# Kernel optimization log

Hardware: AMD Instinct MI355X
Metric: run time of the kernel (lower is better)

## Reference

```python
import jax, jax.numpy as jnp
import numpy as np
import math

B, S, H, DK, NB = 2, 128, 4, 128, 4
D = H * DK  # 512


def setup_inputs() -> dict:
    key = jax.random.key(0)
    ks = jax.random.split(key, 24)
    g = lambda i, sh, std=1.0: jax.random.normal(ks[i], sh, jnp.float32) * std
    u = lambda i, sh: jax.random.uniform(ks[i], sh, jnp.float32)
    return {
        "x_m": g(0, (B, S, D)), "x_c": g(1, (B, S, D)),
        "b_m": g(2, (B, S, D)), "b_c": g(3, (B, S, D)),
        "bb_m": g(4, (B, NB, NB, D)), "bb_c": u(5, (B, NB, NB, D)),
        "p_m": g(6, (B, S, D)), "p_c": u(7, (B, S, D)),
        "W_xm": g(8, (3, D, H, DK), 0.02), "W_xc": g(9, (3, D, H, DK), 0.02),
        "W_bm": g(10, (3, D, H, DK), 0.02), "W_bc": g(11, (3, D, H, DK), 0.02),
        "Wq1_w": g(12, (DK, DK), 0.05), "Wq1_b": g(13, (DK,), 0.02),
        "Wq2_w": g(14, (DK, DK), 0.05), "Wq2_b": g(15, (DK,), 0.02),
        "Wk1_w": g(16, (DK, DK), 0.05), "Wk1_b": g(17, (DK,), 0.02),
        "Wk2_w": g(18, (DK, DK), 0.05), "Wk2_b": g(19, (DK,), 0.02),
        "mean_w": g(20, (D, D), 0.02), "mean_b": jnp.zeros((D,), jnp.float32),
        "cov_w": g(21, (D, D), 0.02), "cov_b": jnp.zeros((D,), jnp.float32),
        "ln_w": jnp.ones((D,), jnp.float32), "ln_b": jnp.zeros((D,), jnp.float32),
        "b_seq": jax.random.randint(ks[22], (B, S), 0, NB),
    }


def _elu1(x):
    return jax.nn.elu(x) + 1.0


def _tri_sagp(m1, m2, m3, c1, c2, c3):
    # fuse three diagonal Gaussians by product-of-Gaussians (precision-weighted)
    eps = 1e-24
    p1 = 1.0 / jnp.clip(c1, eps)
    p2 = 1.0 / jnp.clip(c2, eps)
    p3 = 1.0 / jnp.clip(c3, eps)
    c = 1.0 / (p1 + p2 + p3)
    return c * (m1 * p1 + m2 * p2 + m3 * p3), c


def _ln(x, w, b):
    m = jnp.mean(x, -1, keepdims=True)
    v = jnp.mean((x - m) ** 2, -1, keepdims=True)
    return (x - m) / jnp.sqrt(v + 1e-12) * w + b


def _forward(x_m, x_c, b_m, b_c, bb_m, bb_c, p_m, p_c,
             W_xm, W_xc, W_bm, W_bc,
             Wq1_w, Wq1_b, Wq2_w, Wq2_b, Wk1_w, Wk1_b, Wk2_w, Wk2_b,
             mean_w, mean_b, cov_w, cov_b, ln_w, ln_b, b_seq):
    Bb, Ss, Dd = x_m.shape
    Hh, Dk = W_xm.shape[2], W_xm.shape[3]
    proj = lambda x, w: jnp.einsum('bnd,dhk->bhnk', x, w)
    q1 = proj(x_m, W_xm[0]) + proj(b_m, W_bm[0])
    k1 = proj(x_m, W_xm[1]) + proj(b_m, W_bm[1])
    v1 = proj(x_m, W_xm[2]) + proj(b_m, W_bm[2])
    q2 = _elu1(proj(x_c, W_xc[0]) + proj(b_c, W_bc[0]))
    k2 = _elu1(proj(x_c, W_xc[1]) + proj(b_c, W_bc[1]))
    v2 = _elu1(proj(x_c, W_xc[2]) + proj(b_c, W_bc[2]))
    nb = bb_m.shape[1]
    # [B,NB,NB,D] -> [B,H,NB,NB,DK]
    bbm = bb_m.reshape(Bb, nb, nb, Hh, Dk).transpose(0, 3, 1, 2, 4)
    bbc = bb_c.reshape(Bb, nb, nb, Hh, Dk).transpose(0, 3, 1, 2, 4)
    # out[b,h,i,j,:] = bbm[b,h,b_seq[b,j],b_seq[b,i],:]  (matches torch advanced indexing + permute)
    gather = jax.vmap(lambda bb, seq: bb[:, seq[None, :], seq[:, None], :])
    bbm_b = gather(bbm, b_seq)  # [B,H,S,S,DK]
    bbc_b = gather(bbc, b_seq)
    pm = p_m.reshape(Bb, Ss, Hh, Dk).transpose(0, 2, 1, 3)  # [B,H,S,DK]
    pc = p_c.reshape(Bb, Ss, Hh, Dk).transpose(0, 2, 1, 3)
    lin = lambda x, w, b: x @ w.T + b
    fQm, fQc = _tri_sagp(q1[:, :, :, None, :], lin(bbm_b, Wq1_w, Wq1_b),
                         lin(pm, Wq2_w, Wq2_b)[:, :, :, None, :],
                         q2[:, :, :, None, :], bbc_b, pc[:, :, :, None, :])
    fKm, fKc = _tri_sagp(k1[:, :, None, :, :], lin(bbm_b, Wk1_w, Wk1_b),
                         lin(pm, Wk2_w, Wk2_b)[:, :, None, :, :],
                         k2[:, :, None, :, :], bbc_b, pc[:, :, None, :, :])
    eps = 1e-24
    # 2-Wasserstein^2 between diagonal Gaussians (the 1x1 matmul form reduces to this)
    w2 = jnp.sum((fQm - fKm) ** 2, -1) + jnp.sum(
        (jnp.sqrt(jnp.clip(fQc, eps)) - jnp.sqrt(jnp.clip(fKc, eps))) ** 2, -1)
    scores = -w2 / math.sqrt(Dk)  # [B,H,S,S]
    probs = jax.nn.softmax(scores, axis=-1)
    mean_ctx = jnp.einsum('bhij,bhjk->bhik', probs, v1)
    cov_ctx = jnp.einsum('bhij,bhjk->bhik', probs ** 2, v2)
    mean_ctx = mean_ctx.transpose(0, 2, 1, 3).reshape(Bb, Ss, Dd)
    cov_ctx = cov_ctx.transpose(0, 2, 1, 3).reshape(Bb, Ss, Dd)
    mean_h = _ln(mean_ctx @ mean_w.T + mean_b + x_m, ln_w, ln_b)
    cov_h = _ln(cov_ctx @ cov_w.T + cov_b + x_c, ln_w, ln_b)
    return mean_h, cov_h, probs


def reference(x_m, x_c, b_m, b_c, bb_m, bb_c, p_m, p_c,
              W_xm, W_xc, W_bm, W_bc,
              Wq1_w, Wq1_b, Wq2_w, Wq2_b, Wk1_w, Wk1_b, Wk2_w, Wk2_b,
              mean_w, mean_b, cov_w, cov_b, ln_w, ln_b, b_seq):
    return _forward(x_m, x_c, b_m, b_c, bb_m, bb_c, p_m, p_c,
                    W_xm, W_xc, W_bm, W_bc,
                    Wq1_w, Wq1_b, Wq2_w, Wq2_b, Wk1_w, Wk1_b, Wk2_w, Wk2_b,
                    mean_w, mean_b, cov_w, cov_b, ln_w, ln_b, b_seq)
```

## Files before the change

### kernel.cpp

```cpp
#include <hip/hip_runtime.h>
#include <math.h>

#define B_ 2
#define S_ 128
#define H_ 4
#define DK_ 128
#define NB_ 4
#define D_ 512
#define M_ 256

typedef __attribute__((ext_vector_type(8))) short short8;
typedef __attribute__((ext_vector_type(4))) float float4v;
typedef __attribute__((ext_vector_type(4))) unsigned short ushort4v;

__device__ __forceinline__ float elu1(float x) {
    return (x > 0.f) ? (x + 1.f) : __expf(x);
}

__device__ __forceinline__ unsigned short f2bf(float f) {
    unsigned u = __float_as_uint(f);
    unsigned r = (u + 0x7FFFu + ((u >> 16) & 1u)) >> 16;
    return (unsigned short)r;
}


union __attribute__((aligned(16))) PrepSMem {
    unsigned short tile[32][33];
    struct { float ps[2][8][128]; float wsh[2][128][33]; } c;
};

__global__ __launch_bounds__(256) void k_prep(
    const float* __restrict__ x_m, const float* __restrict__ b_m,
    const float* __restrict__ x_c, const float* __restrict__ b_c,
    const float* __restrict__ mean_w, const float* __restrict__ cov_w,
    const float* __restrict__ W_xm, const float* __restrict__ W_xc,
    const float* __restrict__ W_bm, const float* __restrict__ W_bc,
    const float* __restrict__ p_m, const float* __restrict__ bb_m,
    const float* __restrict__ Wq2, const float* __restrict__ bq2,
    const float* __restrict__ Wk2, const float* __restrict__ bk2,
    const float* __restrict__ Wq1, const float* __restrict__ bq1,
    const float* __restrict__ Wk1, const float* __restrict__ bk1,
    unsigned short* __restrict__ A_m, unsigned short* __restrict__ A_c,
    unsigned short* __restrict__ wm_bf, unsigned short* __restrict__ wc_bf,
    unsigned short* __restrict__ Wt,
    float* __restrict__ pq, float* __restrict__ pk,
    float* __restrict__ bbq, float* __restrict__ bbk)
{
    __shared__ PrepSMem sm;
    const int t = threadIdx.x;
    const int blk = blockIdx.x;
    const int u2 = t >> 7, tl = t & 127;

    {
#pragma unroll
        for (int u = 0; u < 4; ++u) {
            int cid = u * 65536 + blk * 256 + t;
            int job = cid >> 16;
            int off = (cid & 65535) * 4;
            const float* srcp;
            unsigned short* dst;
            if (job <= 1) {
                int m = off >> 10, k = off & 1023;
                if (job == 0) { srcp = (k < 512) ? (x_m + m * 512 + k) : (b_m + m * 512 + k - 512); dst = A_m; }
                else          { srcp = (k < 512) ? (x_c + m * 512 + k) : (b_c + m * 512 + k - 512); dst = A_c; }
            } else if (job == 2) { srcp = mean_w + off; dst = wm_bf; }
            else                 { srcp = cov_w + off;  dst = wc_bf; }
            float4 v = *(const float4*)srcp;
            ushort4v o;
            o.x = f2bf(v.x); o.y = f2bf(v.y); o.z = f2bf(v.z); o.w = f2bf(v.w);
            *(ushort4v*)(dst + off) = o;
        }
    }
    {
        const int tx = t & 31, ty = t >> 5;
        for (int it = 0; it < 12; ++it) {
            int tid = blk * 12 + it;
            int nt = tid & 15, kt = (tid >> 4) & 15, z = tid >> 8;
            int o = z >> 1, part = z & 1;
            const float* src;
            if (part == 0) src = (o < 3) ? (W_xm + o * 262144) : (W_xc + (o - 3) * 262144);
            else           src = (o < 3) ? (W_bm + o * 262144) : (W_bc + (o - 3) * 262144);
            __syncthreads();
#pragma unroll
            for (int u = 0; u < 4; ++u)
                sm.tile[ty + u * 8][tx] = f2bf(src[(kt * 32 + ty + u * 8) * 512 + nt * 32 + tx]);
            __syncthreads();
            unsigned short* dst = Wt + o * 524288 + part * 512;
#pragma unroll
            for (int u = 0; u < 4; ++u)
                dst[(nt * 32 + ty + u * 8) * 1024 + kt * 32 + tx] = sm.tile[tx][ty + u * 8];
        }
    }
    __syncthreads();
    if (blk < 144) {
        const int cunit = blk * 2 + u2;
        const float *src, *Wm, *bias; float* dst; int row0;
        if (cunit < 128)      { src = p_m;  Wm = Wq2; bias = bq2; dst = pq;  row0 = cunit * 8; }
        else if (cunit < 256) { src = p_m;  Wm = Wk2; bias = bk2; dst = pk;  row0 = (cunit - 128) * 8; }
        else if (cunit < 272) { src = bb_m; Wm = Wq1; bias = bq1; dst = bbq; row0 = (cunit - 256) * 8; }
        else                  { src = bb_m; Wm = Wk1; bias = bk1; dst = bbk; row0 = (cunit - 272) * 8; }

        float (*ps)[128] = sm.c.ps[u2];
        float (*wsh)[33] = sm.c.wsh[u2];
#pragma unroll
        for (int r = 0; r < 8; ++r) ps[r][tl] = src[(row0 + r) * 128 + tl];

        float acc[8];
#pragma unroll
        for (int r = 0; r < 8; ++r) acc[r] = 0.f;

        const int kc = tl & 31, kr0 = tl >> 5;
        for (int c0 = 0; c0 < 128; c0 += 32) {
            __syncthreads();
#pragma unroll 8
            for (int u = 0; u < 32; ++u)
                wsh[kr0 + u * 4][kc] = Wm[(kr0 + u * 4) * 128 + c0 + kc];
            __syncthreads();
#pragma unroll 8
            for (int k2 = 0; k2 < 32; ++k2) {
                float wvv = wsh[tl][k2];
#pragma unroll
                for (int r = 0; r < 8; ++r)
                    acc[r] = fmaf(ps[r][c0 + k2], wvv, acc[r]);
            }
        }
        float bv = bias[tl];
#pragma unroll
        for (int r = 0; r < 8; ++r) dst[(row0 + r) * 128 + tl] = acc[r] + bv;
    }
}

__global__ __launch_bounds__(256) void k_mm(
    const unsigned short* __restrict__ A_m, const unsigned short* __restrict__ A_c,
    const unsigned short* __restrict__ Wt, float* __restrict__ qkv)
{
    const int t = threadIdx.x;
    const int wid = blockIdx.x * 4 + (t >> 6);
    const int lane = t & 63;
    const int o = wid >> 9;
    const int rem = wid & 511;
    const int nt = rem & 31, mt = rem >> 5;
    const int m0 = mt * 16, n0 = nt * 16;
    const int l15 = lane & 15, quad = lane >> 4;

    const unsigned short* A = (o < 3) ? A_m : A_c;
    const unsigned short* ap = A + (m0 + l15) * 1024 + quad * 8;
    const unsigned short* bp = Wt + o * 524288 + (n0 + l15) * 1024 + quad * 8;

    float4v acc0 = {0.f, 0.f, 0.f, 0.f};
    float4v acc1 = {0.f, 0.f, 0.f, 0.f};
#pragma unroll
    for (int k0 = 0; k0 < 1024; k0 += 64) {
        short8 a0 = *(const short8*)(ap + k0);
        short8 b0 = *(const short8*)(bp + k0);
        short8 a1 = *(const short8*)(ap + k0 + 32);
        short8 b1 = *(const short8*)(bp + k0 + 32);
        acc0 = __builtin_amdgcn_mfma_f32_16x16x32_bf16(a0, b0, acc0, 0, 0, 0);
        acc1 = __builtin_amdgcn_mfma_f32_16x16x32_bf16(a1, b1, acc1, 0, 0, 0);
    }

    float* dst = qkv + o * 131072;
#pragma unroll
    for (int r = 0; r < 4; ++r) {
        float v = acc0[r] + acc1[r];
        if (o >= 3) v = elu1(v);
        dst[(m0 + quad * 4 + r) * 512 + n0 + l15] = v;
    }
}

__global__ __launch_bounds__(128) void k_fuseK(
    const float* __restrict__ qkv, const float* __restrict__ pk,
    const float* __restrict__ bbk, const float* __restrict__ bb_c,
    const float* __restrict__ p_c, const int* __restrict__ b_seq,
    float* __restrict__ fKm, float* __restrict__ fKs)
{
    const int t = threadIdx.x;
    const int j = blockIdx.x, h = blockIdx.y, b = blockIdx.z;
    const int d = h * 128 + t;
    const float eps = 1e-24f;
    const int base = (b * S_ + j) * D_ + d;
    const int sj = b_seq[b * S_ + j];

    float m1 = qkv[M_ * D_ + base];
    float c1 = qkv[4 * M_ * D_ + base];
    float m3 = pk[base];
    float c3 = p_c[base];

    float p1 = 1.f / fmaxf(c1, eps);
    float p3 = 1.f / fmaxf(c3, eps);
    float mp13 = m1 * p1 + m3 * p3;

#pragma unroll
    for (int sv = 0; sv < 4; ++sv) {
        int idx = (b * 16 + sj * 4 + sv) * 512 + d;
        float m2 = bbk[idx];
        float c2 = bb_c[idx];
        float p2 = 1.f / fmaxf(c2, eps);
        float cc = 1.f / (p1 + p2 + p3);
        int o = (((b * H_ + h) * 4 + sv) * S_ + j) * 128 + t;
        fKm[o] = cc * (mp13 + m2 * p2);
        fKs[o] = sqrtf(fmaxf(cc, eps));
    }
}

__global__ __launch_bounds__(128) void k_attn3(
    const float* __restrict__ qkv, const float* __restrict__ pq,
    const float* __restrict__ bbq, const float* __restrict__ bb_c,
    const float* __restrict__ p_c, const int* __restrict__ b_seq,
    const float* __restrict__ fKm, const float* __restrict__ fKs,
    float* __restrict__ probs_out, unsigned short* __restrict__ mctxb,
    unsigned short* __restrict__ cctxb)
{
    const int t = threadIdx.x;
    const int i = blockIdx.x, h = blockIdx.y, b = blockIdx.z;
    const float eps = 1e-24f;

    __shared__ __attribute__((aligned(16))) float qm[4 * 132];
    __shared__ __attribute__((aligned(16))) float qs[4 * 132];
    __shared__ float red[4];
    __shared__ float pr[128], pr2[128];

    const int si = b_seq[b * S_ + i];
    const int sj = b_seq[b * S_ + t];

    {
        const int d = h * 128 + t;
        const int base = (b * S_ + i) * D_ + d;
        float m1 = qkv[base];
        float c1 = qkv[3 * M_ * D_ + base];
        float m3 = pq[base];
        float c3 = p_c[base];
        float p1 = 1.f / fmaxf(c1, eps);
        float p3 = 1.f / fmaxf(c3, eps);
        float mp13 = m1 * p1 + m3 * p3;
#pragma unroll
        for (int sv = 0; sv < 4; ++sv) {
            int idx = (b * 16 + sv * 4 + si) * 512 + d;
            float m2 = bbq[idx];
            float c2 = bb_c[idx];
            float p2 = 1.f / fmaxf(c2, eps);
            float cc = 1.f / (p1 + p2 + p3);
            qm[sv * 132 + t] = cc * (mp13 + m2 * p2);
            qs[sv * 132 + t] = sqrtf(fmaxf(cc, eps));
        }
    }
    __syncthreads();

    const int krow = (((b * H_ + h) * 4 + si) * S_ + t) * 128;
    const float4* kmp = (const float4*)(fKm + krow);
    const float4* ksp = (const float4*)(fKs + krow);

    float w2 = 0.f;
#pragma unroll 4
    for (int k4 = 0; k4 < 32; ++k4) {
        float4 km = kmp[k4];
        float4 ks = ksp[k4];
        float4 m = *(const float4*)&qm[sj * 132 + k4 * 4];
        float4 s = *(const float4*)&qs[sj * 132 + k4 * 4];
        float d0 = m.x - km.x, d1 = m.y - km.y, d2 = m.z - km.z, d3 = m.w - km.w;
        float e0 = s.x - ks.x, e1 = s.y - ks.y, e2 = s.z - ks.z, e3 = s.w - ks.w;
        w2 += d0 * d0 + d1 * d1 + d2 * d2 + d3 * d3
            + e0 * e0 + e1 * e1 + e2 * e2 + e3 * e3;
    }
    float score = -w2 * 0.08838834764831845f;

    float mx = score;
#pragma unroll
    for (int off = 32; off >= 1; off >>= 1) mx = fmaxf(mx, __shfl_xor(mx, off));
    if ((t & 63) == 0) red[t >> 6] = mx;
    __syncthreads();
    mx = fmaxf(red[0], red[1]);
    float e = __expf(score - mx);
    float sm = e;
#pragma unroll
    for (int off = 32; off >= 1; off >>= 1) sm += __shfl_xor(sm, off);
    if ((t & 63) == 0) red[2 + (t >> 6)] = sm;
    __syncthreads();
    float p = e / (red[2] + red[3]);

    probs_out[((b * H_ + h) * S_ + i) * S_ + t] = p;
    pr[t] = p;
    pr2[t] = p * p;
    __syncthreads();

    const float* v1 = qkv + 2 * M_ * D_ + (b * S_) * D_ + h * 128 + t;
    const float* v2 = qkv + 5 * M_ * D_ + (b * S_) * D_ + h * 128 + t;
    float am = 0.f, ac = 0.f;
#pragma unroll 8
    for (int j = 0; j < 128; ++j) {
        am = fmaf(pr[j], v1[j * D_], am);
        ac = fmaf(pr2[j], v2[j * D_], ac);
    }
    mctxb[(b * S_ + i) * D_ + h * 128 + t] = f2bf(am);
    cctxb[(b * S_ + i) * D_ + h * 128 + t] = f2bf(ac);
}

__global__ __launch_bounds__(256) void k_fin_mm(
    const unsigned short* __restrict__ mctxb, const unsigned short* __restrict__ cctxb,
    const unsigned short* __restrict__ wm_bf, const unsigned short* __restrict__ wc_bf,
    float* __restrict__ y_m, float* __restrict__ y_c)
{
    const int t = threadIdx.x;
    const int wid = blockIdx.x * 4 + (t >> 6);
    const int lane = t & 63;
    const int mat = wid >> 9;
    const int rem = wid & 511;
    const int nt = rem & 31, mt = rem >> 5;
    const int m0 = mt * 16, n0 = nt * 16;
    const int l15 = lane & 15, quad = lane >> 4;

    const unsigned short* A = mat ? cctxb : mctxb;
    const unsigned short* Bw = mat ? wc_bf : wm_bf;
    float* y = mat ? y_c : y_m;

    const unsigned short* ap = A + (m0 + l15) * 512 + quad * 8;
    const unsigned short* bp = Bw + (n0 + l15) * 512 + quad * 8;

    float4v acc0 = {0.f, 0.f, 0.f, 0.f};
    float4v acc1 = {0.f, 0.f, 0.f, 0.f};
#pragma unroll
    for (int k0 = 0; k0 < 512; k0 += 64) {
        short8 a0 = *(const short8*)(ap + k0);
        short8 b0 = *(const short8*)(bp + k0);
        short8 a1 = *(const short8*)(ap + k0 + 32);
        short8 b1 = *(const short8*)(bp + k0 + 32);
        acc0 = __builtin_amdgcn_mfma_f32_16x16x32_bf16(a0, b0, acc0, 0, 0, 0);
        acc1 = __builtin_amdgcn_mfma_f32_16x16x32_bf16(a1, b1, acc1, 0, 0, 0);
    }
#pragma unroll
    for (int r = 0; r < 4; ++r)
        y[(m0 + quad * 4 + r) * 512 + n0 + l15] = acc0[r] + acc1[r];
}

__global__ __launch_bounds__(256) void k_ln(
    const float* __restrict__ y_m, const float* __restrict__ y_c,
    const float* __restrict__ mean_b, const float* __restrict__ cov_b,
    const float* __restrict__ x_m, const float* __restrict__ x_c,
    const float* __restrict__ ln_w, const float* __restrict__ ln_b,
    float* __restrict__ out)
{
    const int t = threadIdx.x;
    const int id = blockIdx.x;
    const int mat = id >> 8, row = id & 255;
    const float* yg = mat ? y_c : y_m;
    const float* bias = mat ? cov_b : mean_b;
    const float* res = mat ? x_c : x_m;
    const int base = row * 512;

    __shared__ float red[8];

    float y0 = yg[base + t] + bias[t] + res[base + t];
    float y1 = yg[base + 256 + t] + bias[256 + t] + res[base + 256 + t];
    float s = y0 + y1, ss = y0 * y0 + y1 * y1;
#pragma unroll
    for (int off = 32; off >= 1; off >>= 1) { s += __shfl_xor(s, off); ss += __shfl_xor(ss, off); }
    if ((t & 63) == 0) { red[t >> 6] = s; red[4 + (t >> 6)] = ss; }
    __syncthreads();
    float mu = (red[0] + red[1] + red[2] + red[3]) * (1.f / 512.f);
    float var = (red[4] + red[5] + red[6] + red[7]) * (1.f / 512.f) - mu * mu;
    float rstd = 1.f / sqrtf(var + 1e-12f);
    out[mat * 131072 + base + t] = (y0 - mu) * rstd * ln_w[t] + ln_b[t];
    out[mat * 131072 + base + 256 + t] = (y1 - mu) * rstd * ln_w[256 + t] + ln_b[256 + t];
}

extern "C" void kernel_launch(void* const* d_in, const int* in_sizes, int n_in,
                              void* d_out, int out_size, void* d_ws, size_t ws_size,
                              hipStream_t stream) {
    (void)in_sizes; (void)n_in; (void)out_size; (void)ws_size;
    const float* x_m   = (const float*)d_in[0];
    const float* x_c   = (const float*)d_in[1];
    const float* b_m   = (const float*)d_in[2];
    const float* b_c   = (const float*)d_in[3];
    const float* bb_m  = (const float*)d_in[4];
    const float* bb_c  = (const float*)d_in[5];
    const float* p_m   = (const float*)d_in[6];
    const float* p_c   = (const float*)d_in[7];
    const float* W_xm  = (const float*)d_in[8];
    const float* W_xc  = (const float*)d_in[9];
    const float* W_bm  = (const float*)d_in[10];
    const float* W_bc  = (const float*)d_in[11];
    const float* Wq1_w = (const float*)d_in[12];
    const float* Wq1_b = (const float*)d_in[13];
    const float* Wq2_w = (const float*)d_in[14];
    const float* Wq2_b = (const float*)d_in[15];
    const float* Wk1_w = (const float*)d_in[16];
    const float* Wk1_b = (const float*)d_in[17];
    const float* Wk2_w = (const float*)d_in[18];
    const float* Wk2_b = (const float*)d_in[19];
    const float* mean_w = (const float*)d_in[20];
    const float* mean_b = (const float*)d_in[21];
    const float* cov_w  = (const float*)d_in[22];
    const float* cov_b  = (const float*)d_in[23];
    const float* ln_w   = (const float*)d_in[24];
    const float* ln_b   = (const float*)d_in[25];
    const int*   b_seq  = (const int*)d_in[26];

    float* ws = (float*)d_ws;
    float* qkv = ws;
    float* pq  = ws + 786432;
    float* pk  = ws + 917504;
    float* bbq = ws + 1048576;
    float* bbk = ws + 1064960;
    float* fKm = ws + 1081344;
    float* fKs = ws + 1605632;
    float* y_m = ws + 2129920;
    float* y_c = ws + 2260992;
    unsigned short* A_m   = (unsigned short*)(ws + 2392064);
    unsigned short* A_c   = (unsigned short*)(ws + 2523136);
    unsigned short* Wt    = (unsigned short*)(ws + 2654208);
    unsigned short* wm_bf = (unsigned short*)(ws + 4227072);
    unsigned short* wc_bf = (unsigned short*)(ws + 4358144);
    unsigned short* mctxb = (unsigned short*)(ws + 4489216);
    unsigned short* cctxb = (unsigned short*)(ws + 4554752);
    float* out = (float*)d_out;

    k_prep<<<dim3(256), 256, 0, stream>>>(
        x_m, b_m, x_c, b_c, mean_w, cov_w, W_xm, W_xc, W_bm, W_bc,
        p_m, bb_m, Wq2_w, Wq2_b, Wk2_w, Wk2_b, Wq1_w, Wq1_b, Wk1_w, Wk1_b,
        A_m, A_c, wm_bf, wc_bf, Wt, pq, pk, bbq, bbk);
    k_mm<<<dim3(768), 256, 0, stream>>>(A_m, A_c, Wt, qkv);
    k_fuseK<<<dim3(128, 4, 2), 128, 0, stream>>>(
        qkv, pk, bbk, bb_c, p_c, b_seq, fKm, fKs);
    k_attn3<<<dim3(128, 4, 2), 128, 0, stream>>>(
        qkv, pq, bbq, bb_c, p_c, b_seq, fKm, fKs, out + 262144, mctxb, cctxb);
    k_fin_mm<<<dim3(256), 256, 0, stream>>>(
        mctxb, cctxb, wm_bf, wc_bf, y_m, y_c);
    k_ln<<<dim3(512), 256, 0, stream>>>(
        y_m, y_c, mean_b, cov_b, x_m, x_c, ln_w, ln_b, out);
}
```

Baseline: 191.1 us.

## Merge six kernels into one cooperative persistent kernel with grid syncs

Replaces the six separate kernel launches with a single cooperative kernel that runs each stage in grid-stride loops and separates stages with grid.sync(). The goal is to remove per-launch overhead and inter-kernel gaps, which matter for a pipeline of many small stages. In exchange, grid-wide barriers add cost. The grid is sized to fit at most two resident blocks per CU, and the attention stage now packs two 128-thread units into each 256-thread block. Both of these can change per-stage parallelism and occupancy.

```diff
diff --git a/kernel.cpp b/kernel.cpp
--- a/kernel.cpp
+++ b/kernel.cpp
@@ -1,5 +1,8 @@
 #include <hip/hip_runtime.h>
+#include <hip/hip_cooperative_groups.h>
 #include <math.h>
+
+namespace cg = cooperative_groups;
 
 #define B_ 2
 #define S_ 128
@@ -24,81 +27,77 @@
 }
 
 
-union __attribute__((aligned(16))) PrepSMem {
+struct Args {
+    const float *x_m, *x_c, *b_m, *b_c, *bb_c, *p_m, *p_c, *bb_m;
+    const float *W_xm, *W_xc, *W_bm, *W_bc;
+    const float *Wq1_w, *Wq1_b, *Wq2_w, *Wq2_b, *Wk1_w, *Wk1_b, *Wk2_w, *Wk2_b;
+    const float *mean_w, *mean_b, *cov_w, *cov_b, *ln_w, *ln_b;
+    const int *b_seq;
+    float *qkv, *pq, *pk, *bbq, *bbk, *fKm, *fKs, *y_m, *y_c, *out;
+    unsigned short *A_m, *A_c, *Wt, *wm_bf, *wc_bf, *mctxb, *cctxb;
+};
+
+union __attribute__((aligned(16))) SMem {
     unsigned short tile[32][33];
     struct { float ps[2][8][128]; float wsh[2][128][33]; } c;
+    struct { float qm[2][528]; float qs[2][528]; float red[2][4];
+             float pr[2][128]; float pr2[2][128]; } a;
+    float red8[8];
 };
 
-__global__ __launch_bounds__(256) void k_prep(
-    const float* __restrict__ x_m, const float* __restrict__ b_m,
-    const float* __restrict__ x_c, const float* __restrict__ b_c,
-    const float* __restrict__ mean_w, const float* __restrict__ cov_w,
-    const float* __restrict__ W_xm, const float* __restrict__ W_xc,
-    const float* __restrict__ W_bm, const float* __restrict__ W_bc,
-    const float* __restrict__ p_m, const float* __restrict__ bb_m,
-    const float* __restrict__ Wq2, const float* __restrict__ bq2,
-    const float* __restrict__ Wk2, const float* __restrict__ bk2,
-    const float* __restrict__ Wq1, const float* __restrict__ bq1,
-    const float* __restrict__ Wk1, const float* __restrict__ bk1,
-    unsigned short* __restrict__ A_m, unsigned short* __restrict__ A_c,
-    unsigned short* __restrict__ wm_bf, unsigned short* __restrict__ wc_bf,
-    unsigned short* __restrict__ Wt,
-    float* __restrict__ pq, float* __restrict__ pk,
-    float* __restrict__ bbq, float* __restrict__ bbk)
+__global__ __launch_bounds__(256, 2) void mega(Args g)
 {
-    __shared__ PrepSMem sm;
+    cg::grid_group grid = cg::this_grid();
+    __shared__ SMem sm;
     const int t = threadIdx.x;
     const int blk = blockIdx.x;
+    const int NBK = gridDim.x;
+    const int wv = t >> 6, lane = t & 63;
     const int u2 = t >> 7, tl = t & 127;
-
-    {
-#pragma unroll
-        for (int u = 0; u < 4; ++u) {
-            int cid = u * 65536 + blk * 256 + t;
-            int job = cid >> 16;
-            int off = (cid & 65535) * 4;
-            const float* srcp;
-            unsigned short* dst;
-            if (job <= 1) {
-                int m = off >> 10, k = off & 1023;
-                if (job == 0) { srcp = (k < 512) ? (x_m + m * 512 + k) : (b_m + m * 512 + k - 512); dst = A_m; }
-                else          { srcp = (k < 512) ? (x_c + m * 512 + k) : (b_c + m * 512 + k - 512); dst = A_c; }
-            } else if (job == 2) { srcp = mean_w + off; dst = wm_bf; }
-            else                 { srcp = cov_w + off;  dst = wc_bf; }
-            float4 v = *(const float4*)srcp;
-            ushort4v o;
-            o.x = f2bf(v.x); o.y = f2bf(v.y); o.z = f2bf(v.z); o.w = f2bf(v.w);
-            *(ushort4v*)(dst + off) = o;
-        }
+    const int l15 = lane & 15, quad = lane >> 4;
+    const float eps = 1e-24f;
+
+    for (int cid = blk * 256 + t; cid < 262144; cid += NBK * 256) {
+        int job = cid >> 16;
+        int off = (cid & 65535) * 4;
+        const float* srcp; unsigned short* dst;
+        if (job <= 1) {
+            int m = off >> 10, k = off & 1023;
+            if (job == 0) { srcp = (k < 512) ? (g.x_m + m * 512 + k) : (g.b_m + m * 512 + k - 512); dst = g.A_m; }
+            else          { srcp = (k < 512) ? (g.x_c + m * 512 + k) : (g.b_c + m * 512 + k - 512); dst = g.A_c; }
+        } else if (job == 2) { srcp = g.mean_w + off; dst = g.wm_bf; }
+        else                 { srcp = g.cov_w + off;  dst = g.wc_bf; }
+        float4 v = *(const float4*)srcp;
+        ushort4v o4;
+        o4.x = f2bf(v.x); o4.y = f2bf(v.y); o4.z = f2bf(v.z); o4.w = f2bf(v.w);
+        *(ushort4v*)(dst + off) = o4;
     }
     {
         const int tx = t & 31, ty = t >> 5;
-        for (int it = 0; it < 12; ++it) {
-            int tid = blk * 12 + it;
+        for (int tid = blk; tid < 3072; tid += NBK) {
             int nt = tid & 15, kt = (tid >> 4) & 15, z = tid >> 8;
             int o = z >> 1, part = z & 1;
             const float* src;
-            if (part == 0) src = (o < 3) ? (W_xm + o * 262144) : (W_xc + (o - 3) * 262144);
-            else           src = (o < 3) ? (W_bm + o * 262144) : (W_bc + (o - 3) * 262144);
+            if (part == 0) src = (o < 3) ? (g.W_xm + o * 262144) : (g.W_xc + (o - 3) * 262144);
+            else           src = (o < 3) ? (g.W_bm + o * 262144) : (g.W_bc + (o - 3) * 262144);
             __syncthreads();
 #pragma unroll
             for (int u = 0; u < 4; ++u)
                 sm.tile[ty + u * 8][tx] = f2bf(src[(kt * 32 + ty + u * 8) * 512 + nt * 32 + tx]);
             __syncthreads();
-            unsigned short* dst = Wt + o * 524288 + part * 512;
+            unsigned short* dst = g.Wt + o * 524288 + part * 512;
 #pragma unroll
             for (int u = 0; u < 4; ++u)
                 dst[(nt * 32 + ty + u * 8) * 1024 + kt * 32 + tx] = sm.tile[tx][ty + u * 8];
         }
     }
     __syncthreads();
-    if (blk < 144) {
-        const int cunit = blk * 2 + u2;
+    for (int cunit = blk * 2 + u2; cunit < 288; cunit += NBK * 2) {
         const float *src, *Wm, *bias; float* dst; int row0;
-        if (cunit < 128)      { src = p_m;  Wm = Wq2; bias = bq2; dst = pq;  row0 = cunit * 8; }
-        else if (cunit < 256) { src = p_m;  Wm = Wk2; bias = bk2; dst = pk;  row0 = (cunit - 128) * 8; }
-        else if (cunit < 272) { src = bb_m; Wm = Wq1; bias = bq1; dst = bbq; row0 = (cunit - 256) * 8; }
-        else                  { src = bb_m; Wm = Wk1; bias = bk1; dst = bbk; row0 = (cunit - 272) * 8; }
+        if (cunit < 128)      { src = g.p_m;  Wm = g.Wq2_w; bias = g.Wq2_b; dst = g.pq;  row0 = cunit * 8; }
+        else if (cunit < 256) { src = g.p_m;  Wm = g.Wk2_w; bias = g.Wk2_b; dst = g.pk;  row0 = (cunit - 128) * 8; }
+        else if (cunit < 272) { src = g.bb_m; Wm = g.Wq1_w; bias = g.Wq1_b; dst = g.bbq; row0 = (cunit - 256) * 8; }
+        else                  { src = g.bb_m; Wm = g.Wk1_w; bias = g.Wk1_b; dst = g.bbk; row0 = (cunit - 272) * 8; }
 
         float (*ps)[128] = sm.c.ps[u2];
         float (*wsh)[33] = sm.c.wsh[u2];
@@ -128,303 +127,271 @@
 #pragma unroll
         for (int r = 0; r < 8; ++r) dst[(row0 + r) * 128 + tl] = acc[r] + bv;
     }
-}
-
-__global__ __launch_bounds__(256) void k_mm(
-    const unsigned short* __restrict__ A_m, const unsigned short* __restrict__ A_c,
-    const unsigned short* __restrict__ Wt, float* __restrict__ qkv)
-{
-    const int t = threadIdx.x;
-    const int wid = blockIdx.x * 4 + (t >> 6);
-    const int lane = t & 63;
-    const int o = wid >> 9;
-    const int rem = wid & 511;
-    const int nt = rem & 31, mt = rem >> 5;
-    const int m0 = mt * 16, n0 = nt * 16;
-    const int l15 = lane & 15, quad = lane >> 4;
-
-    const unsigned short* A = (o < 3) ? A_m : A_c;
-    const unsigned short* ap = A + (m0 + l15) * 1024 + quad * 8;
-    const unsigned short* bp = Wt + o * 524288 + (n0 + l15) * 1024 + quad * 8;
-
-    float4v acc0 = {0.f, 0.f, 0.f, 0.f};
-    float4v acc1 = {0.f, 0.f, 0.f, 0.f};
-#pragma unroll
-    for (int k0 = 0; k0 < 1024; k0 += 64) {
-        short8 a0 = *(const short8*)(ap + k0);
-        short8 b0 = *(const short8*)(bp + k0);
-        short8 a1 = *(const short8*)(ap + k0 + 32);
-        short8 b1 = *(const short8*)(bp + k0 + 32);
-        acc0 = __builtin_amdgcn_mfma_f32_16x16x32_bf16(a0, b0, acc0, 0, 0, 0);
-        acc1 = __builtin_amdgcn_mfma_f32_16x16x32_bf16(a1, b1, acc1, 0, 0, 0);
-    }
-
-    float* dst = qkv + o * 131072;
-#pragma unroll
-    for (int r = 0; r < 4; ++r) {
-        float v = acc0[r] + acc1[r];
-        if (o >= 3) v = elu1(v);
-        dst[(m0 + quad * 4 + r) * 512 + n0 + l15] = v;
-    }
-}
-
-__global__ __launch_bounds__(128) void k_fuseK(
-    const float* __restrict__ qkv, const float* __restrict__ pk,
-    const float* __restrict__ bbk, const float* __restrict__ bb_c,
-    const float* __restrict__ p_c, const int* __restrict__ b_seq,
-    float* __restrict__ fKm, float* __restrict__ fKs)
-{
-    const int t = threadIdx.x;
-    const int j = blockIdx.x, h = blockIdx.y, b = blockIdx.z;
-    const int d = h * 128 + t;
-    const float eps = 1e-24f;
-    const int base = (b * S_ + j) * D_ + d;
-    const int sj = b_seq[b * S_ + j];
-
-    float m1 = qkv[M_ * D_ + base];
-    float c1 = qkv[4 * M_ * D_ + base];
-    float m3 = pk[base];
-    float c3 = p_c[base];
-
-    float p1 = 1.f / fmaxf(c1, eps);
-    float p3 = 1.f / fmaxf(c3, eps);
-    float mp13 = m1 * p1 + m3 * p3;
-
-#pragma unroll
-    for (int sv = 0; sv < 4; ++sv) {
-        int idx = (b * 16 + sj * 4 + sv) * 512 + d;
-        float m2 = bbk[idx];
-        float c2 = bb_c[idx];
-        float p2 = 1.f / fmaxf(c2, eps);
-        float cc = 1.f / (p1 + p2 + p3);
-        int o = (((b * H_ + h) * 4 + sv) * S_ + j) * 128 + t;
-        fKm[o] = cc * (mp13 + m2 * p2);
-        fKs[o] = sqrtf(fmaxf(cc, eps));
-    }
-}
-
-__global__ __launch_bounds__(128) void k_attn3(
-    const float* __restrict__ qkv, const float* __restrict__ pq,
-    const float* __restrict__ bbq, const float* __restrict__ bb_c,
-    const float* __restrict__ p_c, const int* __restrict__ b_seq,
-    const float* __restrict__ fKm, const float* __restrict__ fKs,
-    float* __restrict__ probs_out, unsigned short* __restrict__ mctxb,
-    unsigned short* __restrict__ cctxb)
-{
-    const int t = threadIdx.x;
-    const int i = blockIdx.x, h = blockIdx.y, b = blockIdx.z;
-    const float eps = 1e-24f;
-
-    __shared__ __attribute__((aligned(16))) float qm[4 * 132];
-    __shared__ __attribute__((aligned(16))) float qs[4 * 132];
-    __shared__ float red[4];
-    __shared__ float pr[128], pr2[128];
-
-    const int si = b_seq[b * S_ + i];
-    const int sj = b_seq[b * S_ + t];
-
-    {
-        const int d = h * 128 + t;
-        const int base = (b * S_ + i) * D_ + d;
-        float m1 = qkv[base];
-        float c1 = qkv[3 * M_ * D_ + base];
-        float m3 = pq[base];
-        float c3 = p_c[base];
+
+    grid.sync();
+
+    for (int wid = blk * 4 + wv; wid < 3072; wid += NBK * 4) {
+        int o = wid >> 9;
+        int rem = wid & 511;
+        int nt = rem & 31, mt = rem >> 5;
+        int m0 = mt * 16, n0 = nt * 16;
+
+        const unsigned short* A = (o < 3) ? g.A_m : g.A_c;
+        const unsigned short* ap = A + (m0 + l15) * 1024 + quad * 8;
+        const unsigned short* bp = g.Wt + o * 524288 + (n0 + l15) * 1024 + quad * 8;
+
+        float4v acc0 = {0.f, 0.f, 0.f, 0.f};
+        float4v acc1 = {0.f, 0.f, 0.f, 0.f};
+#pragma unroll
+        for (int k0 = 0; k0 < 1024; k0 += 64) {
+            short8 a0 = *(const short8*)(ap + k0);
+            short8 b0 = *(const short8*)(bp + k0);
+            short8 a1 = *(const short8*)(ap + k0 + 32);
+            short8 b1 = *(const short8*)(bp + k0 + 32);
+            acc0 = __builtin_amdgcn_mfma_f32_16x16x32_bf16(a0, b0, acc0, 0, 0, 0);
+            acc1 = __builtin_amdgcn_mfma_f32_16x16x32_bf16(a1, b1, acc1, 0, 0, 0);
+        }
+        float* dst = g.qkv + o * 131072;
+#pragma unroll
+        for (int r = 0; r < 4; ++r) {
+            float v = acc0[r] + acc1[r];
+            if (o >= 3) v = elu1(v);
+            dst[(m0 + quad * 4 + r) * 512 + n0 + l15] = v;
+        }
+    }
+
+    grid.sync();
+
+    for (int unit = blk * 2 + u2; unit < 1024; unit += NBK * 2) {
+        int j = unit & 127, h = (unit >> 7) & 3, b = unit >> 9;
+        int d = h * 128 + tl;
+        int base = (b * S_ + j) * D_ + d;
+        int sj = g.b_seq[b * S_ + j];
+
+        float m1 = g.qkv[M_ * D_ + base];
+        float c1 = g.qkv[4 * M_ * D_ + base];
+        float m3 = g.pk[base];
+        float c3 = g.p_c[base];
+
         float p1 = 1.f / fmaxf(c1, eps);
         float p3 = 1.f / fmaxf(c3, eps);
         float mp13 = m1 * p1 + m3 * p3;
+
 #pragma unroll
         for (int sv = 0; sv < 4; ++sv) {
-            int idx = (b * 16 + sv * 4 + si) * 512 + d;
-            float m2 = bbq[idx];
-            float c2 = bb_c[idx];
+            int idx = (b * 16 + sj * 4 + sv) * 512 + d;
+            float m2 = g.bbk[idx];
+            float c2 = g.bb_c[idx];
             float p2 = 1.f / fmaxf(c2, eps);
             float cc = 1.f / (p1 + p2 + p3);
-            qm[sv * 132 + t] = cc * (mp13 + m2 * p2);
-            qs[sv * 132 + t] = sqrtf(fmaxf(cc, eps));
-        }
-    }
-    __syncthreads();
-
-    const int krow = (((b * H_ + h) * 4 + si) * S_ + t) * 128;
-    const float4* kmp = (const float4*)(fKm + krow);
-    const float4* ksp = (const float4*)(fKs + krow);
-
-    float w2 = 0.f;
+            int o = (((b * H_ + h) * 4 + sv) * S_ + j) * 128 + tl;
+            g.fKm[o] = cc * (mp13 + m2 * p2);
+            g.fKs[o] = sqrtf(fmaxf(cc, eps));
+        }
+    }
+
+    grid.sync();
+
+    {
+        float* qm = sm.a.qm[u2];
+        float* qs = sm.a.qs[u2];
+        float* red = sm.a.red[u2];
+        float* pr = sm.a.pr[u2];
+        float* pr2 = sm.a.pr2[u2];
+
+        for (int unit = blk * 2 + u2; unit < 1024; unit += NBK * 2) {
+            int i = unit & 127, h = (unit >> 7) & 3, b = unit >> 9;
+
+            __syncthreads();
+            const int si = g.b_seq[b * S_ + i];
+            const int sj = g.b_seq[b * S_ + tl];
+
+            {
+                const int d = h * 128 + tl;
+                const int base = (b * S_ + i) * D_ + d;
+                float m1 = g.qkv[base];
+                float c1 = g.qkv[3 * M_ * D_ + base];
+                float m3 = g.pq[base];
+                float c3 = g.p_c[base];
+                float p1 = 1.f / fmaxf(c1, eps);
+                float p3 = 1.f / fmaxf(c3, eps);
+                float mp13 = m1 * p1 + m3 * p3;
+#pragma unroll
+                for (int sv = 0; sv < 4; ++sv) {
+                    int idx = (b * 16 + sv * 4 + si) * 512 + d;
+                    float m2 = g.bbq[idx];
+                    float c2 = g.bb_c[idx];
+                    float p2 = 1.f / fmaxf(c2, eps);
+                    float cc = 1.f / (p1 + p2 + p3);
+                    qm[sv * 132 + tl] = cc * (mp13 + m2 * p2);
+                    qs[sv * 132 + tl] = sqrtf(fmaxf(cc, eps));
+                }
+            }
+            __syncthreads();
+
+            const int krow = (((b * H_ + h) * 4 + si) * S_ + tl) * 128;
+            const float4* kmp = (const float4*)(g.fKm + krow);
+            const float4* ksp = (const float4*)(g.fKs + krow);
+
+            float w2 = 0.f;
 #pragma unroll 4
-    for (int k4 = 0; k4 < 32; ++k4) {
-        float4 km = kmp[k4];
-        float4 ks = ksp[k4];
-        float4 m = *(const float4*)&qm[sj * 132 + k4 * 4];
-        float4 s = *(const float4*)&qs[sj * 132 + k4 * 4];
-        float d0 = m.x - km.x, d1 = m.y - km.y, d2 = m.z - km.z, d3 = m.w - km.w;
-        float e0 = s.x - ks.x, e1 = s.y - ks.y, e2 = s.z - ks.z, e3 = s.w - ks.w;
-        w2 += d0 * d0 + d1 * d1 + d2 * d2 + d3 * d3
-            + e0 * e0 + e1 * e1 + e2 * e2 + e3 * e3;
-    }
-    float score = -w2 * 0.08838834764831845f;
-
-    float mx = score;
-#pragma unroll
-    for (int off = 32; off >= 1; off >>= 1) mx = fmaxf(mx, __shfl_xor(mx, off));
-    if ((t & 63) == 0) red[t >> 6] = mx;
-    __syncthreads();
-    mx = fmaxf(red[0], red[1]);
-    float e = __expf(score - mx);
-    float sm = e;
-#pragma unroll
-    for (int off = 32; off >= 1; off >>= 1) sm += __shfl_xor(sm, off);
-    if ((t & 63) == 0) red[2 + (t >> 6)] = sm;
-    __syncthreads();
-    float p = e / (red[2] + red[3]);
-
-    probs_out[((b * H_ + h) * S_ + i) * S_ + t] = p;
-    pr[t] = p;
-    pr2[t] = p * p;
-    __syncthreads();
-
-    const float* v1 = qkv + 2 * M_ * D_ + (b * S_) * D_ + h * 128 + t;
-    const float* v2 = qkv + 5 * M_ * D_ + (b * S_) * D_ + h * 128 + t;
-    float am = 0.f, ac = 0.f;
+            for (int k4 = 0; k4 < 32; ++k4) {
+                float4 km = kmp[k4];
+                float4 ks = ksp[k4];
+                float4 m = *(const float4*)&qm[sj * 132 + k4 * 4];
+                float4 s = *(const float4*)&qs[sj * 132 + k4 * 4];
+                float d0 = m.x - km.x, d1 = m.y - km.y, d2 = m.z - km.z, d3 = m.w - km.w;
+                float e0 = s.x - ks.x, e1 = s.y - ks.y, e2 = s.z - ks.z, e3 = s.w - ks.w;
+                w2 += d0 * d0 + d1 * d1 + d2 * d2 + d3 * d3
+                    + e0 * e0 + e1 * e1 + e2 * e2 + e3 * e3;
+            }
+            float score = -w2 * 0.08838834764831845f;
+
+            float mx = score;
+#pragma unroll
+            for (int off = 32; off >= 1; off >>= 1) mx = fmaxf(mx, __shfl_xor(mx, off));
+            if ((tl & 63) == 0) red[tl >> 6] = mx;
+            __syncthreads();
+            mx = fmaxf(red[0], red[1]);
+            float e = __expf(score - mx);
+            float smv = e;
+#pragma unroll
+            for (int off = 32; off >= 1; off >>= 1) smv += __shfl_xor(smv, off);
+            if ((tl & 63) == 0) red[2 + (tl >> 6)] = smv;
+            __syncthreads();
+            float p = e / (red[2] + red[3]);
+
+            g.out[262144 + ((b * H_ + h) * S_ + i) * S_ + tl] = p;
+            pr[tl] = p;
+            pr2[tl] = p * p;
+            __syncthreads();
+
+            const float* v1 = g.qkv + 2 * M_ * D_ + (b * S_) * D_ + h * 128 + tl;
+            const float* v2 = g.qkv + 5 * M_ * D_ + (b * S_) * D_ + h * 128 + tl;
+            float am = 0.f, ac = 0.f;
 #pragma unroll 8
-    for (int j = 0; j < 128; ++j) {
-        am = fmaf(pr[j], v1[j * D_], am);
-        ac = fmaf(pr2[j], v2[j * D_], ac);
-    }
-    mctxb[(b * S_ + i) * D_ + h * 128 + t] = f2bf(am);
-    cctxb[(b * S_ + i) * D_ + h * 128 + t] = f2bf(ac);
-}
-
-__global__ __launch_bounds__(256) void k_fin_mm(
-    const unsigned short* __restrict__ mctxb, const unsigned short* __restrict__ cctxb,
-    const unsigned short* __restrict__ wm_bf, const unsigned short* __restrict__ wc_bf,
-    float* __restrict__ y_m, float* __restrict__ y_c)
-{
-    const int t = threadIdx.x;
-    const int wid = blockIdx.x * 4 + (t >> 6);
-    const int lane = t & 63;
-    const int mat = wid >> 9;
-    const int rem = wid & 511;
-    const int nt = rem & 31, mt = rem >> 5;
-    const int m0 = mt * 16, n0 = nt * 16;
-    const int l15 = lane & 15, quad = lane >> 4;
-
-    const unsigned short* A = mat ? cctxb : mctxb;
-    const unsigned short* Bw = mat ? wc_bf : wm_bf;
-    float* y = mat ? y_c : y_m;
-
-    const unsigned short* ap = A + (m0 + l15) * 512 + quad * 8;
-    const unsigned short* bp = Bw + (n0 + l15) * 512 + quad * 8;
-
-    float4v acc0 = {0.f, 0.f, 0.f, 0.f};
-    float4v acc1 = {0.f, 0.f, 0.f, 0.f};
-#pragma unroll
-    for (int k0 = 0; k0 < 512; k0 += 64) {
-        short8 a0 = *(const short8*)(ap + k0);
-        short8 b0 = *(const short8*)(bp + k0);
-        short8 a1 = *(const short8*)(ap + k0 + 32);
-        short8 b1 = *(const short8*)(bp + k0 + 32);
-        acc0 = __builtin_amdgcn_mfma_f32_16x16x32_bf16(a0, b0, acc0, 0, 0, 0);
-        acc1 = __builtin_amdgcn_mfma_f32_16x16x32_bf16(a1, b1, acc1, 0, 0, 0);
-    }
-#pragma unroll
-    for (int r = 0; r < 4; ++r)
-        y[(m0 + quad * 4 + r) * 512 + n0 + l15] = acc0[r] + acc1[r];
-}
-
-__global__ __launch_bounds__(256) void k_ln(
-    const float* __restrict__ y_m, const float* __restrict__ y_c,
-    const float* __restrict__ mean_b, const float* __restrict__ cov_b,
-    const float* __restrict__ x_m, const float* __restrict__ x_c,
-    const float* __restrict__ ln_w, const float* __restrict__ ln_b,
-    float* __restrict__ out)
-{
-    const int t = threadIdx.x;
-    const int id = blockIdx.x;
-    const int mat = id >> 8, row = id & 255;
-    const float* yg = mat ? y_c : y_m;
-    const float* bias = mat ? cov_b : mean_b;
-    const float* res = mat ? x_c : x_m;
-    const int base = row * 512;
-
-    __shared__ float red[8];
-
-    float y0 = yg[base + t] + bias[t] + res[base + t];
-    float y1 = yg[base + 256 + t] + bias[256 + t] + res[base + 256 + t];
-    float s = y0 + y1, ss = y0 * y0 + y1 * y1;
-#pragma unroll
-    for (int off = 32; off >= 1; off >>= 1) { s += __shfl_xor(s, off); ss += __shfl_xor(ss, off); }
-    if ((t & 63) == 0) { red[t >> 6] = s; red[4 + (t >> 6)] = ss; }
-    __syncthreads();
-    float mu = (red[0] + red[1] + red[2] + red[3]) * (1.f / 512.f);
-    float var = (red[4] + red[5] + red[6] + red[7]) * (1.f / 512.f) - mu * mu;
-    float rstd = 1.f / sqrtf(var + 1e-12f);
-    out[mat * 131072 + base + t] = (y0 - mu) * rstd * ln_w[t] + ln_b[t];
-    out[mat * 131072 + base + 256 + t] = (y1 - mu) * rstd * ln_w[256 + t] + ln_b[256 + t];
+            for (int j = 0; j < 128; ++j) {
+                am = fmaf(pr[j], v1[j * D_], am);
+                ac = fmaf(pr2[j], v2[j * D_], ac);
+            }
+            g.mctxb[(b * S_ + i) * D_ + h * 128 + tl] = f2bf(am);
+            g.cctxb[(b * S_ + i) * D_ + h * 128 + tl] = f2bf(ac);
+        }
+    }
+
+    grid.sync();
+
+    for (int wid = blk * 4 + wv; wid < 1024; wid += NBK * 4) {
+        int mat = wid >> 9;
+        int rem = wid & 511;
+        int nt = rem & 31, mt = rem >> 5;
+        int m0 = mt * 16, n0 = nt * 16;
+
+        const unsigned short* A = mat ? g.cctxb : g.mctxb;
+        const unsigned short* Bw = mat ? g.wc_bf : g.wm_bf;
+        float* y = mat ? g.y_c : g.y_m;
+
+        const unsigned short* ap = A + (m0 + l15) * 512 + quad * 8;
+        const unsigned short* bp = Bw + (n0 + l15) * 512 + quad * 8;
+
+        float4v acc0 = {0.f, 0.f, 0.f, 0.f};
+        float4v acc1 = {0.f, 0.f, 0.f, 0.f};
+#pragma unroll
+        for (int k0 = 0; k0 < 512; k0 += 64) {
+            short8 a0 = *(const short8*)(ap + k0);
+            short8 b0 = *(const short8*)(bp + k0);
+            short8 a1 = *(const short8*)(ap + k0 + 32);
+            short8 b1 = *(const short8*)(bp + k0 + 32);
+            acc0 = __builtin_amdgcn_mfma_f32_16x16x32_bf16(a0, b0, acc0, 0, 0, 0);
+            acc1 = __builtin_amdgcn_mfma_f32_16x16x32_bf16(a1, b1, acc1, 0, 0, 0);
+        }
+#pragma unroll
+        for (int r = 0; r < 4; ++r)
+            y[(m0 + quad * 4 + r) * 512 + n0 + l15] = acc0[r] + acc1[r];
+    }
+
+    grid.sync();
+
+    for (int id = blk; id < 512; id += NBK) {
+        int mat = id >> 8, row = id & 255;
+        const float* yg = mat ? g.y_c : g.y_m;
+        const float* bias = mat ? g.cov_b : g.mean_b;
+        const float* res = mat ? g.x_c : g.x_m;
+        const int base = row * 512;
+
+        float y0 = yg[base + t] + bias[t] + res[base + t];
+        float y1 = yg[base + 256 + t] + bias[256 + t] + res[base + 256 + t];
+        float s = y0 + y1, ss = y0 * y0 + y1 * y1;
+#pragma unroll
+        for (int off = 32; off >= 1; off >>= 1) { s += __shfl_xor(s, off); ss += __shfl_xor(ss, off); }
+        if ((t & 63) == 0) { sm.red8[t >> 6] = s; sm.red8[4 + (t >> 6)] = ss; }
+        __syncthreads();
+        float mu = (sm.red8[0] + sm.red8[1] + sm.red8[2] + sm.red8[3]) * (1.f / 512.f);
+        float var = (sm.red8[4] + sm.red8[5] + sm.red8[6] + sm.red8[7]) * (1.f / 512.f) - mu * mu;
+        float rstd = 1.f / sqrtf(var + 1e-12f);
+        g.out[mat * 131072 + base + t] = (y0 - mu) * rstd * g.ln_w[t] + g.ln_b[t];
+        g.out[mat * 131072 + base + 256 + t] = (y1 - mu) * rstd * g.ln_w[256 + t] + g.ln_b[256 + t];
+        __syncthreads();
+    }
 }
 
 extern "C" void kernel_launch(void* const* d_in, const int* in_sizes, int n_in,
                               void* d_out, int out_size, void* d_ws, size_t ws_size,
                               hipStream_t stream) {
     (void)in_sizes; (void)n_in; (void)out_size; (void)ws_size;
-    const float* x_m   = (const float*)d_in[0];
-    const float* x_c   = (const float*)d_in[1];
-    const float* b_m   = (const float*)d_in[2];
-    const float* b_c   = (const float*)d_in[3];
-    const float* bb_m  = (const float*)d_in[4];
-    const float* bb_c  = (const float*)d_in[5];
-    const float* p_m   = (const float*)d_in[6];
-    const float* p_c   = (const float*)d_in[7];
-    const float* W_xm  = (const float*)d_in[8];
-    const float* W_xc  = (const float*)d_in[9];
-    const float* W_bm  = (const float*)d_in[10];
-    const float* W_bc  = (const float*)d_in[11];
-    const float* Wq1_w = (const float*)d_in[12];
-    const float* Wq1_b = (const float*)d_in[13];
-    const float* Wq2_w = (const float*)d_in[14];
-    const float* Wq2_b = (const float*)d_in[15];
-    const float* Wk1_w = (const float*)d_in[16];
-    const float* Wk1_b = (const float*)d_in[17];
-    const float* Wk2_w = (const float*)d_in[18];
-    const float* Wk2_b = (const float*)d_in[19];
-    const float* mean_w = (const float*)d_in[20];
-    const float* mean_b = (const float*)d_in[21];
-    const float* cov_w  = (const float*)d_in[22];
-    const float* cov_b  = (const float*)d_in[23];
-    const float* ln_w   = (const float*)d_in[24];
-    const float* ln_b   = (const float*)d_in[25];
-    const int*   b_seq  = (const int*)d_in[26];
-
     float* ws = (float*)d_ws;
-    float* qkv = ws;
-    float* pq  = ws + 786432;
-    float* pk  = ws + 917504;
-    float* bbq = ws + 1048576;
-    float* bbk = ws + 1064960;
-    float* fKm = ws + 1081344;
-    float* fKs = ws + 1605632;
-    float* y_m = ws + 2129920;
-    float* y_c = ws + 2260992;
-    unsigned short* A_m   = (unsigned short*)(ws + 2392064);
-    unsigned short* A_c   = (unsigned short*)(ws + 2523136);
-    unsigned short* Wt    = (unsigned short*)(ws + 2654208);
-    unsigned short* wm_bf = (unsigned short*)(ws + 4227072);
-    unsigned short* wc_bf = (unsigned short*)(ws + 4358144);
-    unsigned short* mctxb = (unsigned short*)(ws + 4489216);
-    unsigned short* cctxb = (unsigned short*)(ws + 4554752);
-    float* out = (float*)d_out;
-
-    k_prep<<<dim3(256), 256, 0, stream>>>(
-        x_m, b_m, x_c, b_c, mean_w, cov_w, W_xm, W_xc, W_bm, W_bc,
-        p_m, bb_m, Wq2_w, Wq2_b, Wk2_w, Wk2_b, Wq1_w, Wq1_b, Wk1_w, Wk1_b,
-        A_m, A_c, wm_bf, wc_bf, Wt, pq, pk, bbq, bbk);
-    k_mm<<<dim3(768), 256, 0, stream>>>(A_m, A_c, Wt, qkv);
-    k_fuseK<<<dim3(128, 4, 2), 128, 0, stream>>>(
-        qkv, pk, bbk, bb_c, p_c, b_seq, fKm, fKs);
-    k_attn3<<<dim3(128, 4, 2), 128, 0, stream>>>(
-        qkv, pq, bbq, bb_c, p_c, b_seq, fKm, fKs, out + 262144, mctxb, cctxb);
-    k_fin_mm<<<dim3(256), 256, 0, stream>>>(
-        mctxb, cctxb, wm_bf, wc_bf, y_m, y_c);
-    k_ln<<<dim3(512), 256, 0, stream>>>(
-        y_m, y_c, mean_b, cov_b, x_m, x_c, ln_w, ln_b, out);
+
+    Args a;
+    a.x_m   = (const float*)d_in[0];
+    a.x_c   = (const float*)d_in[1];
+    a.b_m   = (const float*)d_in[2];
+    a.b_c   = (const float*)d_in[3];
+    a.bb_m  = (const float*)d_in[4];
+    a.bb_c  = (const float*)d_in[5];
+    a.p_m   = (const float*)d_in[6];
+    a.p_c   = (const float*)d_in[7];
+    a.W_xm  = (const float*)d_in[8];
+    a.W_xc  = (const float*)d_in[9];
+    a.W_bm  = (const float*)d_in[10];
+    a.W_bc  = (const float*)d_in[11];
+    a.Wq1_w = (const float*)d_in[12];
+    a.Wq1_b = (const float*)d_in[13];
+    a.Wq2_w = (const float*)d_in[14];
+    a.Wq2_b = (const float*)d_in[15];
+    a.Wk1_w = (const float*)d_in[16];
+    a.Wk1_b = (const float*)d_in[17];
+    a.Wk2_w = (const float*)d_in[18];
+    a.Wk2_b = (const float*)d_in[19];
+    a.mean_w = (const float*)d_in[20];
+    a.mean_b = (const float*)d_in[21];
+    a.cov_w  = (const float*)d_in[22];
+    a.cov_b  = (const float*)d_in[23];
+    a.ln_w   = (const float*)d_in[24];
+    a.ln_b   = (const float*)d_in[25];
+    a.b_seq  = (const int*)d_in[26];
+
+    a.qkv = ws;
+    a.pq  = ws + 786432;
+    a.pk  = ws + 917504;
+    a.bbq = ws + 1048576;
+    a.bbk = ws + 1064960;
+    a.fKm = ws + 1081344;
+    a.fKs = ws + 1605632;
+    a.y_m = ws + 2129920;
+    a.y_c = ws + 2260992;
+    a.A_m   = (unsigned short*)(ws + 2392064);
+    a.A_c   = (unsigned short*)(ws + 2523136);
+    a.Wt    = (unsigned short*)(ws + 2654208);
+    a.wm_bf = (unsigned short*)(ws + 4227072);
+    a.wc_bf = (unsigned short*)(ws + 4358144);
+    a.mctxb = (unsigned short*)(ws + 4489216);
+    a.cctxb = (unsigned short*)(ws + 4554752);
+    a.out = (float*)d_out;
+
+    int maxb = 0;
+    hipOccupancyMaxActiveBlocksPerMultiprocessor(&maxb, mega, 256, 0);
+    int nblk = (maxb >= 2) ? 512 : 256;
+
+    void* params[] = { (void*)&a };
+    hipLaunchCooperativeKernel((void*)mega, dim3(nblk), dim3(256), params, 0u, stream);
 }
```

Result: slower. 374.7 us (+96.1%).
